# Kernel tuning notes

Measured on AMD Instinct MI355X. Metric: run time of the kernel, lower is better.

The kernel has to match this reference:

```python
import jax, jax.numpy as jnp
import numpy as np

B, M, S, P, A, D, H = 16, 8, 100, 40, 3, 128, 8
HD = D // H  # head dim = 16
EPS = 1e-5


def _layernorm(x, g, b):
    mu = jnp.mean(x, axis=-1, keepdims=True)
    var = jnp.mean(jnp.square(x - mu), axis=-1, keepdims=True)
    return (x - mu) * jax.lax.rsqrt(var + EPS) * g + b


def setup_inputs() -> dict:
    key = jax.random.key(0)
    ks = jax.random.split(key, 20)
    attrs = jax.random.normal(ks[0], (B, M, S, P, A), dtype=jnp.float32)
    valid = (jax.random.uniform(ks[1], (B, M, S, P)) < 0.85).astype(jnp.float32)
    roads = jnp.concatenate([attrs, valid[..., None]], axis=-1)  # (B,M,S,P,A+1)
    agents_emb = jax.random.normal(ks[2], (4, B, M, D), dtype=jnp.float32)

    def xavier(k, shape):
        fan_in, fan_out = shape[-2], shape[-1]
        std = float(np.sqrt(2.0 / (fan_in + fan_out)))
        return jax.random.normal(k, shape, dtype=jnp.float32) * std

    return {
        "roads": roads,
        "agents_emb": agents_emb,
        "map_seeds": xavier(ks[3], (1, 1, D)),
        "lin_w": xavier(ks[4], (A, D)), "lin_b": jnp.zeros((D,)),
        "wq": xavier(ks[5], (D, D)), "wk": xavier(ks[6], (D, D)), "wv": xavier(ks[7], (D, D)),
        "bq": jnp.zeros((D,)), "bk": jnp.zeros((D,)), "bv": jnp.zeros((D,)),
        "out_w": xavier(ks[8], (D, D)), "out_b": jnp.zeros((D,)),
        "ln1_g": jnp.ones((D,)), "ln1_b": jnp.zeros((D,)),
        "w1": xavier(ks[9], (D, 3 * D)), "b1": jnp.zeros((3 * D,)),
        "w2": xavier(ks[10], (3 * D, D)), "b2": jnp.zeros((D,)),
        "ln2_g": jnp.ones((D,)), "ln2_b": jnp.zeros((D,)),
    }


def reference(roads, agents_emb, map_seeds, lin_w, lin_b, wq, wk, wv, bq, bk, bv,
              out_w, out_b, ln1_g, ln1_b, w1, b1, w2, b2, ln2_g, ln2_b):
    N = B * M * S
    last = roads[..., -1]  # (B,M,S,P), exact 0/1 existence flags
    # --- masks (True = padded / ignore) ---
    seg_mask = jnp.sum(last, axis=3) == 0  # (B,M,S)
    pts_mask = (1.0 - last).astype(bool).reshape(N, P)
    all_pts = jnp.all(pts_mask, axis=-1)
    pts_mask = pts_mask.at[:, 0].set(pts_mask[:, 0] & ~all_pts)  # unmask pt 0 of empty segs
    all_seg = jnp.all(seg_mask, axis=-1)
    seg_mask = seg_mask.at[:, :, 0].set(seg_mask[:, :, 0] & ~all_seg)

    # --- point feature projection ---
    feats = roads[..., :A].reshape(N, P, A) @ lin_w + lin_b  # (N,P,D)

    # --- single-query multi-head attention pooling (eval mode: no dropout) ---
    q = (map_seeds.reshape(D) @ wq + bq).reshape(H, HD)  # shared seed query
    k = (feats @ wk + bk).reshape(N, P, H, HD)
    v = (feats @ wv + bv).reshape(N, P, H, HD)
    scores = jnp.einsum('hd,nphd->nhp', q, k) * (HD ** -0.5)  # (N,H,P)
    scores = jnp.where(pts_mask[:, None, :], -1e9, scores)
    attn = jax.nn.softmax(scores, axis=-1)
    ctx = jnp.einsum('nhp,nphd->nhd', attn, v).reshape(N, D)
    emb = _layernorm(ctx @ out_w + out_b, ln1_g, ln1_b)  # (N,D)

    # --- FFN + residual + norm (eval mode: no dropout) ---
    ffn = jax.nn.relu(emb @ w1 + b1) @ w2 + b2
    emb2 = _layernorm(emb + ffn, ln2_g, ln2_b)

    out = emb2.reshape(B, M, S, D).transpose(2, 0, 1, 3)  # (S,B,M,D)
    return out, seg_mask
```

## Files before the change

kernel.cpp:

```cpp
#include <hip/hip_runtime.h>

namespace {
constexpr int Sn = 100;
constexpr int Nn = 12800;
constexpr int OUT0 = 1638400;
}

using bf16x8 = __attribute__((ext_vector_type(8))) short;
using f32x4  = __attribute__((ext_vector_type(4))) float;
#define MFMA16(a, b, c) __builtin_amdgcn_mfma_f32_16x16x32_bf16((a), (b), (c), 0, 0, 0)

__device__ __forceinline__ unsigned short f2bf(float x) {
  unsigned int u = __float_as_uint(x);
  return (unsigned short)((u + 0x7FFFu + ((u >> 16) & 1u)) >> 16);
}
__device__ __forceinline__ float bf2f(unsigned short h) {
  return __uint_as_float(((unsigned int)h) << 16);
}

__global__ __launch_bounds__(128) void k0_precompute(
    const float* __restrict__ ms, const float* __restrict__ wq,
    const float* __restrict__ wk, const float* __restrict__ bq,
    const float* __restrict__ bk, const float* __restrict__ lin_w,
    const float* __restrict__ lin_b, const float* __restrict__ wv,
    const float* __restrict__ bv, const float* __restrict__ out_w,
    float* __restrict__ W4qk, float* __restrict__ T) {
  const int t = threadIdx.x;
  if (blockIdx.x < 8) {
    const int h = blockIdx.x;
    __shared__ float q[128];
    __shared__ float qkh[128];
    __shared__ float qbkh;
    __shared__ float part[128];
    float s = bq[t];
    for (int c = 0; c < 128; ++c) s += ms[c] * wq[c * 128 + t];
    q[t] = s;
    __syncthreads();
    float a = 0.f;
#pragma unroll
    for (int j = 0; j < 16; ++j) a += q[h * 16 + j] * wk[t * 128 + h * 16 + j];
    qkh[t] = a * 0.25f;
    if (t == 0) {
      float b = 0.f;
#pragma unroll
      for (int j = 0; j < 16; ++j) b += q[h * 16 + j] * bk[h * 16 + j];
      qbkh = b * 0.25f;
    }
    __syncthreads();
    const int j = t >> 5, cp = t & 31;
    float p = 0.f;
    for (int c = cp * 4; c < cp * 4 + 4; ++c) {
      const float w4 = (j < 3) ? lin_w[j * 128 + c] : lin_b[c];
      p += w4 * qkh[c];
    }
    part[t] = p;
    __syncthreads();
    if (t < 4) {
      float sum = 0.f;
      for (int i = 0; i < 32; ++i) sum += part[t * 32 + i];
      if (t == 3) sum += qbkh;
      W4qk[t * 8 + h] = sum;
    }
  } else {
    const int hj = blockIdx.x - 8;
    const int h = hj >> 2, j = hj & 3;
    __shared__ float part[128];
    __shared__ float w4wv[16];
    const int cp = t & 7;
    float p = 0.f;
    for (int c = cp * 16; c < cp * 16 + 16; ++c) {
      const float w4 = (j < 3) ? lin_w[j * 128 + c] : lin_b[c];
      p += w4 * wv[c * 128 + (h * 16 + (t >> 3))];
    }
    part[t] = p;
    __syncthreads();
    if (t < 16) {
      float sum = 0.f;
      for (int i = 0; i < 8; ++i) sum += part[t * 8 + i];
      if (j == 3) sum += bv[h * 16 + t];
      w4wv[t] = sum;
    }
    __syncthreads();
    float acc = 0.f;
#pragma unroll
    for (int e2 = 0; e2 < 16; ++e2) acc += w4wv[e2] * out_w[(h * 16 + e2) * 128 + t];
    T[hj * 128 + t] = acc;
  }
}

__global__ __launch_bounds__(256) void k0b_repack(
    const float* __restrict__ w1, const float* __restrict__ w2,
    const float* __restrict__ T,
    unsigned short* __restrict__ w1f, unsigned short* __restrict__ w2f,
    unsigned short* __restrict__ Tf) {
  const int gid = blockIdx.x * 256 + threadIdx.x;
  const int tile = gid >> 6, lane = gid & 63;
  const int quad = lane >> 4, n16 = lane & 15;
  unsigned short hi[8], lo[8];
  unsigned short* dst;
  if (tile < 96) {
    const int nt = tile >> 2, kk = tile & 3;
    const int n = nt * 16 + n16;
#pragma unroll
    for (int j = 0; j < 8; ++j) {
      const int k = kk * 32 + quad * 8 + j;
      const float v = w1[k * 384 + n];
      hi[j] = f2bf(v); lo[j] = f2bf(v - bf2f(hi[j]));
    }
    dst = w1f + (size_t)tile * 1024 + lane * 8;
  } else if (tile < 192) {
    const int t2 = tile - 96;
    const int nt2 = t2 / 12, kk2 = t2 % 12;
    const int n = nt2 * 16 + n16;
#pragma unroll
    for (int j = 0; j < 8; ++j) {
      const int k = kk2 * 32 + quad * 8 + j;
      const float v = w2[k * 128 + n];
      hi[j] = f2bf(v); lo[j] = f2bf(v - bf2f(hi[j]));
    }
    dst = w2f + (size_t)(tile - 96) * 1024 + lane * 8;
  } else {
    const int nt = tile - 192;
    const int n = nt * 16 + n16;
#pragma unroll
    for (int j = 0; j < 8; ++j) {
      const int k = quad * 8 + j;
      const float v = T[k * 128 + n];
      hi[j] = f2bf(v); lo[j] = f2bf(v - bf2f(hi[j]));
    }
    dst = Tf + (size_t)nt * 1024 + lane * 8;
  }
#pragma unroll
  for (int j = 0; j < 8; ++j) { dst[j] = hi[j]; dst[512 + j] = lo[j]; }
}

__global__ __launch_bounds__(256) void k_all(
    const float* __restrict__ roads, const float* __restrict__ W4qk_g,
    const unsigned short* __restrict__ Tf, const float* __restrict__ out_b,
    const float* __restrict__ ln1_g, const float* __restrict__ ln1_b,
    const unsigned short* __restrict__ w1f, const unsigned short* __restrict__ w2f,
    const float* __restrict__ b1, const float* __restrict__ b2,
    const float* __restrict__ ln2_g, const float* __restrict__ ln2_b,
    float* __restrict__ out) {
  const int t = threadIdx.x;
  const int n0 = blockIdx.x * 16;

  __shared__ union {
    float4 pts[640];
    __align__(16) unsigned short A2[24576];
  } u;
  __shared__ __align__(16) unsigned short A1[4096];
  __shared__ __align__(16) unsigned short ApF[1024];
  __shared__ float w4qk_l[32];
  __shared__ float lnr[16][4][2];

  for (int i = t; i < 640; i += 256)
    u.pts[i] = ((const float4*)roads)[(size_t)n0 * 40 + i];
  if (t < 32) w4qk_l[t] = W4qk_g[t];
  __syncthreads();

  {
    const int sh = t >> 1, seg = sh >> 3, h = sh & 7;
    const int p0 = (t & 1) * 20;
    const float wa = w4qk_l[h], wb = w4qk_l[8 + h];
    const float wc = w4qk_l[16 + h], wd = w4qk_l[24 + h];
    float ax = 0.f, ay = 0.f, az = 0.f, den = 0.f;
    int nv = 0;
    for (int p = p0; p < p0 + 20; ++p) {
      const float4 pt = u.pts[seg * 40 + p];
      if (pt.w != 0.f) {
        const float e = __expf(wd + pt.x * wa + pt.y * wb + pt.z * wc);
        ax += e * pt.x; ay += e * pt.y; az += e * pt.z; den += e; ++nv;
      }
    }
    ax += __shfl_xor(ax, 1); ay += __shfl_xor(ay, 1); az += __shfl_xor(az, 1);
    den += __shfl_xor(den, 1); nv += __shfl_xor(nv, 1);
    if ((t & 1) == 0) {
      if (nv == 0) {
        const float4 z = u.pts[seg * 40];
        ax = z.x; ay = z.y; az = z.z; den = 1.f;
      }
      const float inv = 1.f / den;
      const float v[4] = {ax * inv, ay * inv, az * inv, 1.f};
      ushort4 hi, lo;
      unsigned short* hp = (unsigned short*)&hi;
      unsigned short* lp = (unsigned short*)&lo;
#pragma unroll
      for (int c = 0; c < 4; ++c) { hp[c] = f2bf(v[c]); lp[c] = f2bf(v[c] - bf2f(hp[c])); }
      const int slot = ((h >> 1) * 16 + seg) * 8 + (h & 1) * 4;
      *(ushort4*)&ApF[slot] = hi;
      *(ushort4*)&ApF[512 + slot] = lo;
      if (h == 0) out[OUT0 + n0 + seg] = (nv == 0) ? 1.f : 0.f;
    }
  }
  __syncthreads();

  const int w = t >> 6, lane = t & 63;
  const int quad = lane >> 4, nlane = lane & 15;

  float embv[2][4];
  {
    const bf16x8 ahi = *(const bf16x8*)&ApF[lane * 8];
    const bf16x8 alo = *(const bf16x8*)&ApF[512 + lane * 8];
#pragma unroll
    for (int n2 = 0; n2 < 2; ++n2) {
      const int nt = w * 2 + n2;
      const unsigned short* tp = Tf + (size_t)nt * 1024;
      const bf16x8 bhi = *(const bf16x8*)(tp + lane * 8);
      const bf16x8 blo = *(const bf16x8*)(tp + 512 + lane * 8);
      f32x4 acc = (f32x4){0.f, 0.f, 0.f, 0.f};
      acc = MFMA16(alo, bhi, acc);
      acc = MFMA16(ahi, blo, acc);
      acc = MFMA16(ahi, bhi, acc);
      const float ob = out_b[nt * 16 + nlane];
#pragma unroll
      for (int r = 0; r < 4; ++r) embv[n2][r] = acc[r] + ob;
    }
#pragma unroll
    for (int r = 0; r < 4; ++r) {
      float s = embv[0][r] + embv[1][r];
      float v = embv[0][r] * embv[0][r] + embv[1][r] * embv[1][r];
#pragma unroll
      for (int m = 1; m < 16; m <<= 1) { s += __shfl_xor(s, m); v += __shfl_xor(v, m); }
      if (nlane == 0) { lnr[quad * 4 + r][w][0] = s; lnr[quad * 4 + r][w][1] = v; }
    }
  }
  __syncthreads();
#pragma unroll
  for (int r = 0; r < 4; ++r) {
    const int row = quad * 4 + r;
    const float mu = (lnr[row][0][0] + lnr[row][1][0] + lnr[row][2][0] + lnr[row][3][0]) * (1.f / 128.f);
    const float msq = (lnr[row][0][1] + lnr[row][1][1] + lnr[row][2][1] + lnr[row][3][1]) * (1.f / 128.f);
    const float rstd = rsqrtf(msq - mu * mu + 1e-5f);
#pragma unroll
    for (int n2 = 0; n2 < 2; ++n2) {
      const int col = (w * 2 + n2) * 16 + nlane;
      const float e = (embv[n2][r] - mu) * rstd * ln1_g[col] + ln1_b[col];
      const unsigned short hh = f2bf(e), hl = f2bf(e - bf2f(hh));
      const int kk = col >> 5, q2 = (col >> 3) & 3, j = col & 7;
      const int idx = kk * 512 + (q2 * 16 + row) * 8 + j;
      A1[idx] = hh; A1[2048 + idx] = hl;
    }
  }
  __syncthreads();

#pragma unroll
  for (int nti = 0; nti < 6; ++nti) {
    const int nt = w * 6 + nti;
    f32x4 acc = (f32x4){0.f, 0.f, 0.f, 0.f};
#pragma unroll
    for (int kk = 0; kk < 4; ++kk) {
      const bf16x8 ahi = *(const bf16x8*)&A1[kk * 512 + lane * 8];
      const bf16x8 alo = *(const bf16x8*)&A1[2048 + kk * 512 + lane * 8];
      const unsigned short* wp = w1f + (size_t)(nt * 4 + kk) * 1024;
      const bf16x8 bhi = *(const bf16x8*)(wp + lane * 8);
      const bf16x8 blo = *(const bf16x8*)(wp + 512 + lane * 8);
      acc = MFMA16(alo, bhi, acc);
      acc = MFMA16(ahi, blo, acc);
      acc = MFMA16(ahi, bhi, acc);
    }
    const int col = nt * 16 + nlane;
    const float bias = b1[col];
    const int kk2 = col >> 5, qA = (col >> 3) & 3, jA = col & 7;
#pragma unroll
    for (int r = 0; r < 4; ++r) {
      const float h = fmaxf(acc[r] + bias, 0.f);
      const unsigned short hh = f2bf(h), hl = f2bf(h - bf2f(hh));
      const int idx = kk2 * 512 + (qA * 16 + quad * 4 + r) * 8 + jA;
      u.A2[idx] = hh; u.A2[12288 + idx] = hl;
    }
  }
  __syncthreads();

  f32x4 acc2[2];
  acc2[0] = (f32x4){0.f, 0.f, 0.f, 0.f};
  acc2[1] = (f32x4){0.f, 0.f, 0.f, 0.f};
#pragma unroll 4
  for (int kk2 = 0; kk2 < 12; ++kk2) {
    const bf16x8 ahi = *(const bf16x8*)&u.A2[kk2 * 512 + lane * 8];
    const bf16x8 alo = *(const bf16x8*)&u.A2[12288 + kk2 * 512 + lane * 8];
#pragma unroll
    for (int n2 = 0; n2 < 2; ++n2) {
      const unsigned short* wp = w2f + (size_t)((w * 2 + n2) * 12 + kk2) * 1024;
      const bf16x8 bhi = *(const bf16x8*)(wp + lane * 8);
      const bf16x8 blo = *(const bf16x8*)(wp + 512 + lane * 8);
      acc2[n2] = MFMA16(alo, bhi, acc2[n2]);
      acc2[n2] = MFMA16(ahi, blo, acc2[n2]);
      acc2[n2] = MFMA16(ahi, bhi, acc2[n2]);
    }
  }

  float y[2][4];
#pragma unroll
  for (int n2 = 0; n2 < 2; ++n2) {
    const int col = (w * 2 + n2) * 16 + nlane;
    const float bb = b2[col];
    const int kk = col >> 5, q2 = (col >> 3) & 3, j = col & 7;
#pragma unroll
    for (int r = 0; r < 4; ++r) {
      const int idx = kk * 512 + (q2 * 16 + quad * 4 + r) * 8 + j;
      y[n2][r] = acc2[n2][r] + bb + bf2f(A1[idx]) + bf2f(A1[2048 + idx]);
    }
  }
#pragma unroll
  for (int r = 0; r < 4; ++r) {
    float s = y[0][r] + y[1][r];
    float v = y[0][r] * y[0][r] + y[1][r] * y[1][r];
#pragma unroll
    for (int m = 1; m < 16; m <<= 1) { s += __shfl_xor(s, m); v += __shfl_xor(v, m); }
    if (nlane == 0) { lnr[quad * 4 + r][w][0] = s; lnr[quad * 4 + r][w][1] = v; }
  }
  __syncthreads();
#pragma unroll
  for (int r = 0; r < 4; ++r) {
    const int row = quad * 4 + r;
    const float mu = (lnr[row][0][0] + lnr[row][1][0] + lnr[row][2][0] + lnr[row][3][0]) * (1.f / 128.f);
    const float msq = (lnr[row][0][1] + lnr[row][1][1] + lnr[row][2][1] + lnr[row][3][1]) * (1.f / 128.f);
    const float rstd = rsqrtf(msq - mu * mu + 1e-5f);
    const int n = n0 + row, si = n % 100, bm = n / 100;
#pragma unroll
    for (int n2 = 0; n2 < 2; ++n2) {
      const int col = (w * 2 + n2) * 16 + nlane;
      out[(size_t)si * 16384 + bm * 128 + col] =
          (y[n2][r] - mu) * rstd * ln2_g[col] + ln2_b[col];
    }
  }
}

__global__ void k2_fix_segmask(float* __restrict__ out) {
  const int bm = blockIdx.x, t = threadIdx.x;
  const float* base = out + OUT0 + bm * Sn;
  const float a = base[t];
  const float b = (t < 36) ? base[64 + t] : 0.f;
  const unsigned long long m = __ballot((a != 0.f) || (b != 0.f));
  if (t == 0 && m == 0ULL) out[OUT0 + bm * Sn] = 0.f;
}

extern "C" void kernel_launch(void* const* d_in, const int* in_sizes, int n_in,
                              void* d_out, int out_size, void* d_ws, size_t ws_size,
                              hipStream_t stream) {
  const float* roads = (const float*)d_in[0];
  const float* ms    = (const float*)d_in[2];
  const float* lin_w = (const float*)d_in[3];
  const float* lin_b = (const float*)d_in[4];
  const float* wq    = (const float*)d_in[5];
  const float* wk    = (const float*)d_in[6];
  const float* wv    = (const float*)d_in[7];
  const float* bq    = (const float*)d_in[8];
  const float* bk    = (const float*)d_in[9];
  const float* bv    = (const float*)d_in[10];
  const float* out_w = (const float*)d_in[11];
  const float* out_b = (const float*)d_in[12];
  const float* ln1_g = (const float*)d_in[13];
  const float* ln1_b = (const float*)d_in[14];
  const float* w1    = (const float*)d_in[15];
  const float* b1    = (const float*)d_in[16];
  const float* w2    = (const float*)d_in[17];
  const float* b2    = (const float*)d_in[18];
  const float* ln2_g = (const float*)d_in[19];
  const float* ln2_b = (const float*)d_in[20];

  float* out  = (float*)d_out;
  float* W4qk = (float*)d_ws;
  float* T    = W4qk + 32;
  unsigned short* w1f = (unsigned short*)(T + 4096);
  unsigned short* w2f = w1f + 96 * 1024;
  unsigned short* Tf  = w2f + 96 * 1024;

  k0_precompute<<<40, 128, 0, stream>>>(ms, wq, wk, bq, bk, lin_w, lin_b, wv, bv, out_w, W4qk, T);
  k0b_repack<<<50, 256, 0, stream>>>(w1, w2, T, w1f, w2f, Tf);
  k_all<<<Nn / 16, 256, 0, stream>>>(roads, W4qk, Tf, out_b, ln1_g, ln1_b,
                                     w1f, w2f, b1, b2, ln2_g, ln2_b, out);
  k2_fix_segmask<<<128, 64, 0, stream>>>(out);
}
```

Baseline: 135.1 us.

## Process 32 segments per block and merge weight precompute kernels

The main kernel now handles two 16-row tiles per block, so each weight fragment loaded from global memory feeds two MFMA row tiles and the number of blocks is halved (400 instead of 800). The two setup kernels are merged into one launch: the T precompute writes its split-bf16 fragments directly and skips the intermediate fp32 buffer and the extra launch. This roughly doubles register and LDS use per block, which may lower occupancy, and 400 blocks may underfill the GPU.

Measured after the change: 144.3 us. 6.8% more time.

```diff
diff --git a/kernel.cpp b/kernel.cpp
--- a/kernel.cpp
+++ b/kernel.cpp
@@ -18,120 +18,105 @@
   return __uint_as_float(((unsigned int)h) << 16);
 }
 
-__global__ __launch_bounds__(128) void k0_precompute(
+__global__ __launch_bounds__(256) void k0m(
     const float* __restrict__ ms, const float* __restrict__ wq,
     const float* __restrict__ wk, const float* __restrict__ bq,
     const float* __restrict__ bk, const float* __restrict__ lin_w,
     const float* __restrict__ lin_b, const float* __restrict__ wv,
     const float* __restrict__ bv, const float* __restrict__ out_w,
-    float* __restrict__ W4qk, float* __restrict__ T) {
+    const float* __restrict__ w1, const float* __restrict__ w2,
+    float* __restrict__ W4qk, unsigned short* __restrict__ w1f,
+    unsigned short* __restrict__ w2f, unsigned short* __restrict__ Tf) {
   const int t = threadIdx.x;
-  if (blockIdx.x < 8) {
-    const int h = blockIdx.x;
+  if (blockIdx.x < 48) {
+    const int gid = blockIdx.x * 256 + t;
+    const int tile = gid >> 6, lane = gid & 63;
+    const int quad = lane >> 4, n16 = lane & 15;
+    unsigned short hi[8], lo[8];
+    unsigned short* dst;
+    if (tile < 96) {
+      const int nt = tile >> 2, kk = tile & 3;
+      const int n = nt * 16 + n16;
+#pragma unroll
+      for (int j = 0; j < 8; ++j) {
+        const int k = kk * 32 + quad * 8 + j;
+        const float v = w1[k * 384 + n];
+        hi[j] = f2bf(v); lo[j] = f2bf(v - bf2f(hi[j]));
+      }
+      dst = w1f + (size_t)tile * 1024 + lane * 8;
+    } else {
+      const int t2 = tile - 96;
+      const int nt2 = t2 / 12, kk2 = t2 % 12;
+      const int n = nt2 * 16 + n16;
+#pragma unroll
+      for (int j = 0; j < 8; ++j) {
+        const int k = kk2 * 32 + quad * 8 + j;
+        const float v = w2[k * 128 + n];
+        hi[j] = f2bf(v); lo[j] = f2bf(v - bf2f(hi[j]));
+      }
+      dst = w2f + (size_t)t2 * 1024 + lane * 8;
+    }
+#pragma unroll
+    for (int j = 0; j < 8; ++j) { dst[j] = hi[j]; dst[512 + j] = lo[j]; }
+  } else {
     __shared__ float q[128];
-    __shared__ float qkh[128];
-    __shared__ float qbkh;
-    __shared__ float part[128];
-    float s = bq[t];
-    for (int c = 0; c < 128; ++c) s += ms[c] * wq[c * 128 + t];
-    q[t] = s;
+    __shared__ float qk_s[8][128];
+    __shared__ float qbk_s[8];
+    __shared__ float w4wv_s[32][16];
+    if (t < 128) {
+      float s = bq[t];
+      for (int c = 0; c < 128; ++c) s += ms[c] * wq[c * 128 + t];
+      q[t] = s;
+    }
     __syncthreads();
-    float a = 0.f;
-#pragma unroll
-    for (int j = 0; j < 16; ++j) a += q[h * 16 + j] * wk[t * 128 + h * 16 + j];
-    qkh[t] = a * 0.25f;
-    if (t == 0) {
+    if (t < 128) {
+      for (int h = 0; h < 8; ++h) {
+        float a = 0.f;
+#pragma unroll
+        for (int j = 0; j < 16; ++j) a += q[h * 16 + j] * wk[t * 128 + h * 16 + j];
+        qk_s[h][t] = a * 0.25f;
+      }
+    }
+    if (t < 8) {
       float b = 0.f;
 #pragma unroll
-      for (int j = 0; j < 16; ++j) b += q[h * 16 + j] * bk[h * 16 + j];
-      qbkh = b * 0.25f;
+      for (int j = 0; j < 16; ++j) b += q[t * 16 + j] * bk[t * 16 + j];
+      qbk_s[t] = b * 0.25f;
     }
     __syncthreads();
-    const int j = t >> 5, cp = t & 31;
-    float p = 0.f;
-    for (int c = cp * 4; c < cp * 4 + 4; ++c) {
-      const float w4 = (j < 3) ? lin_w[j * 128 + c] : lin_b[c];
-      p += w4 * qkh[c];
-    }
-    part[t] = p;
+    if (t < 32) {
+      const int j = t >> 3, h = t & 7;
+      float s = 0.f;
+      for (int c = 0; c < 128; ++c) {
+        const float w4 = (j < 3) ? lin_w[j * 128 + c] : lin_b[c];
+        s += w4 * qk_s[h][c];
+      }
+      if (j == 3) s += qbk_s[h];
+      W4qk[j * 8 + h] = s;
+    }
+#pragma unroll
+    for (int ii = t * 2; ii < t * 2 + 2; ++ii) {
+      const int hj = ii >> 4, e = ii & 15, j = hj & 3, h = hj >> 2;
+      float s = 0.f;
+      for (int c = 0; c < 128; ++c) {
+        const float w4 = (j < 3) ? lin_w[j * 128 + c] : lin_b[c];
+        s += w4 * wv[c * 128 + h * 16 + e];
+      }
+      if (j == 3) s += bv[h * 16 + e];
+      w4wv_s[hj][e] = s;
+    }
     __syncthreads();
-    if (t < 4) {
-      float sum = 0.f;
-      for (int i = 0; i < 32; ++i) sum += part[t * 32 + i];
-      if (t == 3) sum += qbkh;
-      W4qk[t * 8 + h] = sum;
-    }
-  } else {
-    const int hj = blockIdx.x - 8;
-    const int h = hj >> 2, j = hj & 3;
-    __shared__ float part[128];
-    __shared__ float w4wv[16];
-    const int cp = t & 7;
-    float p = 0.f;
-    for (int c = cp * 16; c < cp * 16 + 16; ++c) {
-      const float w4 = (j < 3) ? lin_w[j * 128 + c] : lin_b[c];
-      p += w4 * wv[c * 128 + (h * 16 + (t >> 3))];
-    }
-    part[t] = p;
-    __syncthreads();
-    if (t < 16) {
-      float sum = 0.f;
-      for (int i = 0; i < 8; ++i) sum += part[t * 8 + i];
-      if (j == 3) sum += bv[h * 16 + t];
-      w4wv[t] = sum;
-    }
-    __syncthreads();
-    float acc = 0.f;
-#pragma unroll
-    for (int e2 = 0; e2 < 16; ++e2) acc += w4wv[e2] * out_w[(h * 16 + e2) * 128 + t];
-    T[hj * 128 + t] = acc;
-  }
-}
-
-__global__ __launch_bounds__(256) void k0b_repack(
-    const float* __restrict__ w1, const float* __restrict__ w2,
-    const float* __restrict__ T,
-    unsigned short* __restrict__ w1f, unsigned short* __restrict__ w2f,
-    unsigned short* __restrict__ Tf) {
-  const int gid = blockIdx.x * 256 + threadIdx.x;
-  const int tile = gid >> 6, lane = gid & 63;
-  const int quad = lane >> 4, n16 = lane & 15;
-  unsigned short hi[8], lo[8];
-  unsigned short* dst;
-  if (tile < 96) {
-    const int nt = tile >> 2, kk = tile & 3;
-    const int n = nt * 16 + n16;
-#pragma unroll
-    for (int j = 0; j < 8; ++j) {
-      const int k = kk * 32 + quad * 8 + j;
-      const float v = w1[k * 384 + n];
-      hi[j] = f2bf(v); lo[j] = f2bf(v - bf2f(hi[j]));
-    }
-    dst = w1f + (size_t)tile * 1024 + lane * 8;
-  } else if (tile < 192) {
-    const int t2 = tile - 96;
-    const int nt2 = t2 / 12, kk2 = t2 % 12;
-    const int n = nt2 * 16 + n16;
-#pragma unroll
-    for (int j = 0; j < 8; ++j) {
-      const int k = kk2 * 32 + quad * 8 + j;
-      const float v = w2[k * 128 + n];
-      hi[j] = f2bf(v); lo[j] = f2bf(v - bf2f(hi[j]));
-    }
-    dst = w2f + (size_t)(tile - 96) * 1024 + lane * 8;
-  } else {
-    const int nt = tile - 192;
-    const int n = nt * 16 + n16;
-#pragma unroll
-    for (int j = 0; j < 8; ++j) {
-      const int k = quad * 8 + j;
-      const float v = T[k * 128 + n];
-      hi[j] = f2bf(v); lo[j] = f2bf(v - bf2f(hi[j]));
-    }
-    dst = Tf + (size_t)nt * 1024 + lane * 8;
-  }
-#pragma unroll
-  for (int j = 0; j < 8; ++j) { dst[j] = hi[j]; dst[512 + j] = lo[j]; }
+    for (int i = t; i < 4096; i += 256) {
+      const int hj = i >> 7, col = i & 127, h = hj >> 2;
+      float v = 0.f;
+#pragma unroll
+      for (int e = 0; e < 16; ++e) v += w4wv_s[hj][e] * out_w[(h * 16 + e) * 128 + col];
+      const unsigned short hh = f2bf(v), hl = f2bf(v - bf2f(hh));
+      const int nt = col >> 4, lane = ((hj >> 3) << 4) + (col & 15), j = hj & 7;
+      Tf[(size_t)nt * 1024 + lane * 8 + j] = hh;
+      Tf[(size_t)nt * 1024 + 512 + lane * 8 + j] = hl;
+    }
+  }
 }
 
 __global__ __launch_bounds__(256) void k_all(
@@ -143,188 +128,231 @@
     const float* __restrict__ ln2_g, const float* __restrict__ ln2_b,
     float* __restrict__ out) {
   const int t = threadIdx.x;
-  const int n0 = blockIdx.x * 16;
+  const int n0 = blockIdx.x * 32;
 
   __shared__ union {
-    float4 pts[640];
+    float4 pts[1280];
     __align__(16) unsigned short A2[24576];
   } u;
-  __shared__ __align__(16) unsigned short A1[4096];
-  __shared__ __align__(16) unsigned short ApF[1024];
+  __shared__ __align__(16) unsigned short A1[8192];
+  __shared__ __align__(16) unsigned short ApF[2048];
   __shared__ float w4qk_l[32];
-  __shared__ float lnr[16][4][2];
-
-  for (int i = t; i < 640; i += 256)
+  __shared__ float lnr[32][4][2];
+
+  for (int i = t; i < 1280; i += 256)
     u.pts[i] = ((const float4*)roads)[(size_t)n0 * 40 + i];
   if (t < 32) w4qk_l[t] = W4qk_g[t];
   __syncthreads();
 
   {
-    const int sh = t >> 1, seg = sh >> 3, h = sh & 7;
-    const int p0 = (t & 1) * 20;
+    const int seg = t >> 3, h = t & 7;
     const float wa = w4qk_l[h], wb = w4qk_l[8 + h];
     const float wc = w4qk_l[16 + h], wd = w4qk_l[24 + h];
     float ax = 0.f, ay = 0.f, az = 0.f, den = 0.f;
     int nv = 0;
-    for (int p = p0; p < p0 + 20; ++p) {
+    for (int p = 0; p < 40; ++p) {
       const float4 pt = u.pts[seg * 40 + p];
       if (pt.w != 0.f) {
         const float e = __expf(wd + pt.x * wa + pt.y * wb + pt.z * wc);
         ax += e * pt.x; ay += e * pt.y; az += e * pt.z; den += e; ++nv;
       }
     }
-    ax += __shfl_xor(ax, 1); ay += __shfl_xor(ay, 1); az += __shfl_xor(az, 1);
-    den += __shfl_xor(den, 1); nv += __shfl_xor(nv, 1);
-    if ((t & 1) == 0) {
-      if (nv == 0) {
-        const float4 z = u.pts[seg * 40];
-        ax = z.x; ay = z.y; az = z.z; den = 1.f;
-      }
-      const float inv = 1.f / den;
-      const float v[4] = {ax * inv, ay * inv, az * inv, 1.f};
-      ushort4 hi, lo;
-      unsigned short* hp = (unsigned short*)&hi;
-      unsigned short* lp = (unsigned short*)&lo;
-#pragma unroll
-      for (int c = 0; c < 4; ++c) { hp[c] = f2bf(v[c]); lp[c] = f2bf(v[c] - bf2f(hp[c])); }
-      const int slot = ((h >> 1) * 16 + seg) * 8 + (h & 1) * 4;
-      *(ushort4*)&ApF[slot] = hi;
-      *(ushort4*)&ApF[512 + slot] = lo;
-      if (h == 0) out[OUT0 + n0 + seg] = (nv == 0) ? 1.f : 0.f;
-    }
+    if (nv == 0) {
+      const float4 z = u.pts[seg * 40];
+      ax = z.x; ay = z.y; az = z.z; den = 1.f;
+    }
+    const float inv = 1.f / den;
+    const float v[4] = {ax * inv, ay * inv, az * inv, 1.f};
+    const int rt = seg >> 4, m = seg & 15;
+    const int slot = rt * 1024 + (((h >> 1) * 16 + m) * 8 + (h & 1) * 4);
+    ushort4 hi, lo;
+    unsigned short* hp = (unsigned short*)&hi;
+    unsigned short* lp = (unsigned short*)&lo;
+#pragma unroll
+    for (int c = 0; c < 4; ++c) { hp[c] = f2bf(v[c]); lp[c] = f2bf(v[c] - bf2f(hp[c])); }
+    *(ushort4*)&ApF[slot] = hi;
+    *(ushort4*)&ApF[512 + slot] = lo;
+    if (h == 0) out[OUT0 + n0 + seg] = (nv == 0) ? 1.f : 0.f;
   }
   __syncthreads();
 
   const int w = t >> 6, lane = t & 63;
   const int quad = lane >> 4, nlane = lane & 15;
 
-  float embv[2][4];
+  float embv[2][2][4];
   {
-    const bf16x8 ahi = *(const bf16x8*)&ApF[lane * 8];
-    const bf16x8 alo = *(const bf16x8*)&ApF[512 + lane * 8];
+    bf16x8 ah[2], al[2];
+#pragma unroll
+    for (int rt = 0; rt < 2; ++rt) {
+      ah[rt] = *(const bf16x8*)&ApF[rt * 1024 + lane * 8];
+      al[rt] = *(const bf16x8*)&ApF[rt * 1024 + 512 + lane * 8];
+    }
 #pragma unroll
     for (int n2 = 0; n2 < 2; ++n2) {
       const int nt = w * 2 + n2;
       const unsigned short* tp = Tf + (size_t)nt * 1024;
       const bf16x8 bhi = *(const bf16x8*)(tp + lane * 8);
       const bf16x8 blo = *(const bf16x8*)(tp + 512 + lane * 8);
-      f32x4 acc = (f32x4){0.f, 0.f, 0.f, 0.f};
-      acc = MFMA16(alo, bhi, acc);
-      acc = MFMA16(ahi, blo, acc);
-      acc = MFMA16(ahi, bhi, acc);
       const float ob = out_b[nt * 16 + nlane];
 #pragma unroll
-      for (int r = 0; r < 4; ++r) embv[n2][r] = acc[r] + ob;
-    }
+      for (int rt = 0; rt < 2; ++rt) {
+        f32x4 acc = (f32x4){0.f, 0.f, 0.f, 0.f};
+        acc = MFMA16(al[rt], bhi, acc);
+        acc = MFMA16(ah[rt], blo, acc);
+        acc = MFMA16(ah[rt], bhi, acc);
+#pragma unroll
+        for (int r = 0; r < 4; ++r) embv[n2][rt][r] = acc[r] + ob;
+      }
+    }
+#pragma unroll
+    for (int rt = 0; rt < 2; ++rt)
+#pragma unroll
+      for (int r = 0; r < 4; ++r) {
+        float s = embv[0][rt][r] + embv[1][rt][r];
+        float v = embv[0][rt][r] * embv[0][rt][r] + embv[1][rt][r] * embv[1][rt][r];
+#pragma unroll
+        for (int m = 1; m < 16; m <<= 1) { s += __shfl_xor(s, m); v += __shfl_xor(v, m); }
+        if (nlane == 0) {
+          const int row = rt * 16 + quad * 4 + r;
+          lnr[row][w][0] = s; lnr[row][w][1] = v;
+        }
+      }
+  }
+  __syncthreads();
+
+#pragma unroll
+  for (int rt = 0; rt < 2; ++rt)
 #pragma unroll
     for (int r = 0; r < 4; ++r) {
-      float s = embv[0][r] + embv[1][r];
-      float v = embv[0][r] * embv[0][r] + embv[1][r] * embv[1][r];
-#pragma unroll
-      for (int m = 1; m < 16; m <<= 1) { s += __shfl_xor(s, m); v += __shfl_xor(v, m); }
-      if (nlane == 0) { lnr[quad * 4 + r][w][0] = s; lnr[quad * 4 + r][w][1] = v; }
-    }
-  }
-  __syncthreads();
-#pragma unroll
-  for (int r = 0; r < 4; ++r) {
-    const int row = quad * 4 + r;
-    const float mu = (lnr[row][0][0] + lnr[row][1][0] + lnr[row][2][0] + lnr[row][3][0]) * (1.f / 128.f);
-    const float msq = (lnr[row][0][1] + lnr[row][1][1] + lnr[row][2][1] + lnr[row][3][1]) * (1.f / 128.f);
-    const float rstd = rsqrtf(msq - mu * mu + 1e-5f);
-#pragma unroll
-    for (int n2 = 0; n2 < 2; ++n2) {
-      const int col = (w * 2 + n2) * 16 + nlane;
-      const float e = (embv[n2][r] - mu) * rstd * ln1_g[col] + ln1_b[col];
-      const unsigned short hh = f2bf(e), hl = f2bf(e - bf2f(hh));
-      const int kk = col >> 5, q2 = (col >> 3) & 3, j = col & 7;
-      const int idx = kk * 512 + (q2 * 16 + row) * 8 + j;
-      A1[idx] = hh; A1[2048 + idx] = hl;
-    }
-  }
-  __syncthreads();
-
-#pragma unroll
-  for (int nti = 0; nti < 6; ++nti) {
-    const int nt = w * 6 + nti;
-    f32x4 acc = (f32x4){0.f, 0.f, 0.f, 0.f};
-#pragma unroll
-    for (int kk = 0; kk < 4; ++kk) {
-      const bf16x8 ahi = *(const bf16x8*)&A1[kk * 512 + lane * 8];
-      const bf16x8 alo = *(const bf16x8*)&A1[2048 + kk * 512 + lane * 8];
-      const unsigned short* wp = w1f + (size_t)(nt * 4 + kk) * 1024;
-      const bf16x8 bhi = *(const bf16x8*)(wp + lane * 8);
-      const bf16x8 blo = *(const bf16x8*)(wp + 512 + lane * 8);
-      acc = MFMA16(alo, bhi, acc);
-      acc = MFMA16(ahi, blo, acc);
-      acc = MFMA16(ahi, bhi, acc);
-    }
-    const int col = nt * 16 + nlane;
-    const float bias = b1[col];
-    const int kk2 = col >> 5, qA = (col >> 3) & 3, jA = col & 7;
-#pragma unroll
-    for (int r = 0; r < 4; ++r) {
-      const float h = fmaxf(acc[r] + bias, 0.f);
-      const unsigned short hh = f2bf(h), hl = f2bf(h - bf2f(hh));
-      const int idx = kk2 * 512 + (qA * 16 + quad * 4 + r) * 8 + jA;
-      u.A2[idx] = hh; u.A2[12288 + idx] = hl;
-    }
-  }
-  __syncthreads();
-
-  f32x4 acc2[2];
-  acc2[0] = (f32x4){0.f, 0.f, 0.f, 0.f};
-  acc2[1] = (f32x4){0.f, 0.f, 0.f, 0.f};
-#pragma unroll 4
+      const int row = rt * 16 + quad * 4 + r;
+      const float mu = (lnr[row][0][0] + lnr[row][1][0] + lnr[row][2][0] + lnr[row][3][0]) * (1.f / 128.f);
+      const float msq = (lnr[row][0][1] + lnr[row][1][1] + lnr[row][2][1] + lnr[row][3][1]) * (1.f / 128.f);
+      const float rstd = rsqrtf(msq - mu * mu + 1e-5f);
+#pragma unroll
+      for (int n2 = 0; n2 < 2; ++n2) {
+        const int col = (w * 2 + n2) * 16 + nlane;
+        const float e = (embv[n2][rt][r] - mu) * rstd * ln1_g[col] + ln1_b[col];
+        const unsigned short hh = f2bf(e), hl = f2bf(e - bf2f(hh));
+        const int kk = col >> 5, q2 = (col >> 3) & 3, j = col & 7;
+        const int idx = rt * 2048 + kk * 512 + (q2 * 16 + quad * 4 + r) * 8 + j;
+        A1[idx] = hh; A1[4096 + idx] = hl;
+      }
+    }
+  __syncthreads();
+
+  {
+    bf16x8 a1h[2][4], a1l[2][4];
+#pragma unroll
+    for (int rt = 0; rt < 2; ++rt)
+#pragma unroll
+      for (int kk = 0; kk < 4; ++kk) {
+        a1h[rt][kk] = *(const bf16x8*)&A1[rt * 2048 + kk * 512 + lane * 8];
+        a1l[rt][kk] = *(const bf16x8*)&A1[4096 + rt * 2048 + kk * 512 + lane * 8];
+      }
+    for (int nti = 0; nti < 6; ++nti) {
+      const int nt = w * 6 + nti;
+      f32x4 acc[2];
+      acc[0] = (f32x4){0.f, 0.f, 0.f, 0.f};
+      acc[1] = (f32x4){0.f, 0.f, 0.f, 0.f};
+#pragma unroll
+      for (int kk = 0; kk < 4; ++kk) {
+        const unsigned short* wp = w1f + (size_t)(nt * 4 + kk) * 1024;
+        const bf16x8 bhi = *(const bf16x8*)(wp + lane * 8);
+        const bf16x8 blo = *(const bf16x8*)(wp + 512 + lane * 8);
+#pragma unroll
+        for (int rt = 0; rt < 2; ++rt) {
+          acc[rt] = MFMA16(a1l[rt][kk], bhi, acc[rt]);
+          acc[rt] = MFMA16(a1h[rt][kk], blo, acc[rt]);
+          acc[rt] = MFMA16(a1h[rt][kk], bhi, acc[rt]);
+        }
+      }
+      const int col = nt * 16 + nlane;
+      const float bias = b1[col];
+      const int kk2 = col >> 5, qA = (col >> 3) & 3, jA = col & 7;
+#pragma unroll
+      for (int rt = 0; rt < 2; ++rt)
+#pragma unroll
+        for (int r = 0; r < 4; ++r) {
+          const float h = fmaxf(acc[rt][r] + bias, 0.f);
+          const unsigned short hh = f2bf(h), hl = f2bf(h - bf2f(hh));
+          const int idx = rt * 6144 + kk2 * 512 + (qA * 16 + quad * 4 + r) * 8 + jA;
+          u.A2[idx] = hh; u.A2[12288 + idx] = hl;
+        }
+    }
+  }
+  __syncthreads();
+
+  f32x4 acc2[2][2];
+#pragma unroll
+  for (int n2 = 0; n2 < 2; ++n2)
+#pragma unroll
+    for (int rt = 0; rt < 2; ++rt) acc2[n2][rt] = (f32x4){0.f, 0.f, 0.f, 0.f};
+#pragma unroll 3
   for (int kk2 = 0; kk2 < 12; ++kk2) {
-    const bf16x8 ahi = *(const bf16x8*)&u.A2[kk2 * 512 + lane * 8];
-    const bf16x8 alo = *(const bf16x8*)&u.A2[12288 + kk2 * 512 + lane * 8];
+    bf16x8 hh[2], hl[2];
+#pragma unroll
+    for (int rt = 0; rt < 2; ++rt) {
+      hh[rt] = *(const bf16x8*)&u.A2[rt * 6144 + kk2 * 512 + lane * 8];
+      hl[rt] = *(const bf16x8*)&u.A2[12288 + rt * 6144 + kk2 * 512 + lane * 8];
+    }
 #pragma unroll
     for (int n2 = 0; n2 < 2; ++n2) {
       const unsigned short* wp = w2f + (size_t)((w * 2 + n2) * 12 + kk2) * 1024;
       const bf16x8 bhi = *(const bf16x8*)(wp + lane * 8);
       const bf16x8 blo = *(const bf16x8*)(wp + 512 + lane * 8);
-      acc2[n2] = MFMA16(alo, bhi, acc2[n2]);
-      acc2[n2] = MFMA16(ahi, blo, acc2[n2]);
-      acc2[n2] = MFMA16(ahi, bhi, acc2[n2]);
-    }
-  }
-
-  float y[2][4];
+#pragma unroll
+      for (int rt = 0; rt < 2; ++rt) {
+        acc2[n2][rt] = MFMA16(hl[rt], bhi, acc2[n2][rt]);
+        acc2[n2][rt] = MFMA16(hh[rt], blo, acc2[n2][rt]);
+        acc2[n2][rt] = MFMA16(hh[rt], bhi, acc2[n2][rt]);
+      }
+    }
+  }
+
+  float y[2][2][4];
 #pragma unroll
   for (int n2 = 0; n2 < 2; ++n2) {
     const int col = (w * 2 + n2) * 16 + nlane;
     const float bb = b2[col];
     const int kk = col >> 5, q2 = (col >> 3) & 3, j = col & 7;
 #pragma unroll
+    for (int rt = 0; rt < 2; ++rt)
+#pragma unroll
+      for (int r = 0; r < 4; ++r) {
+        const int idx = rt * 2048 + kk * 512 + (q2 * 16 + quad * 4 + r) * 8 + j;
+        y[n2][rt][r] = acc2[n2][rt][r] + bb + bf2f(A1[idx]) + bf2f(A1[4096 + idx]);
+      }
+  }
+#pragma unroll
+  for (int rt = 0; rt < 2; ++rt)
+#pragma unroll
     for (int r = 0; r < 4; ++r) {
-      const int idx = kk * 512 + (q2 * 16 + quad * 4 + r) * 8 + j;
-      y[n2][r] = acc2[n2][r] + bb + bf2f(A1[idx]) + bf2f(A1[2048 + idx]);
-    }
-  }
-#pragma unroll
-  for (int r = 0; r < 4; ++r) {
-    float s = y[0][r] + y[1][r];
-    float v = y[0][r] * y[0][r] + y[1][r] * y[1][r];
-#pragma unroll
-    for (int m = 1; m < 16; m <<= 1) { s += __shfl_xor(s, m); v += __shfl_xor(v, m); }
-    if (nlane == 0) { lnr[quad * 4 + r][w][0] = s; lnr[quad * 4 + r][w][1] = v; }
-  }
-  __syncthreads();
-#pragma unroll
-  for (int r = 0; r < 4; ++r) {
-    const int row = quad * 4 + r;
-    const float mu = (lnr[row][0][0] + lnr[row][1][0] + lnr[row][2][0] + lnr[row][3][0]) * (1.f / 128.f);
-    const float msq = (lnr[row][0][1] + lnr[row][1][1] + lnr[row][2][1] + lnr[row][3][1]) * (1.f / 128.f);
-    const float rstd = rsqrtf(msq - mu * mu + 1e-5f);
-    const int n = n0 + row, si = n % 100, bm = n / 100;
-#pragma unroll
-    for (int n2 = 0; n2 < 2; ++n2) {
-      const int col = (w * 2 + n2) * 16 + nlane;
-      out[(size_t)si * 16384 + bm * 128 + col] =
-          (y[n2][r] - mu) * rstd * ln2_g[col] + ln2_b[col];
-    }
-  }
+      float s = y[0][rt][r] + y[1][rt][r];
+      float v = y[0][rt][r] * y[0][rt][r] + y[1][rt][r] * y[1][rt][r];
+#pragma unroll
+      for (int m = 1; m < 16; m <<= 1) { s += __shfl_xor(s, m); v += __shfl_xor(v, m); }
+      if (nlane == 0) {
+        const int row = rt * 16 + quad * 4 + r;
+        lnr[row][w][0] = s; lnr[row][w][1] = v;
+      }
+    }
+  __syncthreads();
+#pragma unroll
+  for (int rt = 0; rt < 2; ++rt)
+#pragma unroll
+    for (int r = 0; r < 4; ++r) {
+      const int row = rt * 16 + quad * 4 + r;
+      const float mu = (lnr[row][0][0] + lnr[row][1][0] + lnr[row][2][0] + lnr[row][3][0]) * (1.f / 128.f);
+      const float msq = (lnr[row][0][1] + lnr[row][1][1] + lnr[row][2][1] + lnr[row][3][1]) * (1.f / 128.f);
+      const float rstd = rsqrtf(msq - mu * mu + 1e-5f);
+      const int n = n0 + row, si = n % 100, bm = n / 100;
+#pragma unroll
+      for (int n2 = 0; n2 < 2; ++n2) {
+        const int col = (w * 2 + n2) * 16 + nlane;
+        out[(size_t)si * 16384 + bm * 128 + col] =
+            (y[n2][rt][r] - mu) * rstd * ln2_g[col] + ln2_b[col];
+      }
+    }
 }
 
 __global__ void k2_fix_segmask(float* __restrict__ out) {
@@ -362,14 +390,13 @@
 
   float* out  = (float*)d_out;
   float* W4qk = (float*)d_ws;
-  float* T    = W4qk + 32;
-  unsigned short* w1f = (unsigned short*)(T + 4096);
+  unsigned short* w1f = (unsigned short*)(W4qk + 32);
   unsigned short* w2f = w1f + 96 * 1024;
   unsigned short* Tf  = w2f + 96 * 1024;
 
-  k0_precompute<<<40, 128, 0, stream>>>(ms, wq, wk, bq, bk, lin_w, lin_b, wv, bv, out_w, W4qk, T);
-  k0b_repack<<<50, 256, 0, stream>>>(w1, w2, T, w1f, w2f, Tf);
-  k_all<<<Nn / 16, 256, 0, stream>>>(roads, W4qk, Tf, out_b, ln1_g, ln1_b,
+  k0m<<<49, 256, 0, stream>>>(ms, wq, wk, bq, bk, lin_w, lin_b, wv, bv, out_w,
+                              w1, w2, W4qk, w1f, w2f, Tf);
+  k_all<<<Nn / 32, 256, 0, stream>>>(roads, W4qk, Tf, out_b, ln1_g, ln1_b,
                                      w1f, w2f, b1, b2, ln2_g, ln2_b, out);
   k2_fix_segmask<<<128, 64, 0, stream>>>(out);
 }
```
